# Optimization experiments

Hardware: AMD Instinct MI355X
Metric: run time of the kernel (lower is better)

## Reference

```python
import jax, jax.numpy as jnp
import numpy as np

B, H, W, C, HEADS, WS, SS = 32, 56, 56, 512, 16, 7, 3
HID = 4 * C
N = WS * WS          # tokens per window = 49
NW = (H // WS) * (W // WS)  # windows per image = 64
HD = C // HEADS
SCALE = HD ** -0.5

def _rel_index():
    coords = np.stack(np.meshgrid(np.arange(WS), np.arange(WS), indexing='ij'))
    cf = coords.reshape(2, -1)
    rel = (cf[:, :, None] - cf[:, None, :]).transpose(1, 2, 0)
    rel[..., 0] += WS - 1
    rel[..., 1] += WS - 1
    rel[..., 0] *= 2 * WS - 1
    return rel.sum(-1)  # [N, N]

REL_IDX = _rel_index()

def _attn_mask():
    # standard Swin SW-MSA mask: label 3x3 shifted regions, diff labels -> -100
    img = np.zeros((H, W), dtype=np.float32)
    cnt = 0
    for hs in (slice(0, -WS), slice(-WS, -SS), slice(-SS, None)):
        for ws_ in (slice(0, -WS), slice(-WS, -SS), slice(-SS, None)):
            img[hs, ws_] = cnt
            cnt += 1
    mw = img.reshape(H // WS, WS, W // WS, WS).transpose(0, 2, 1, 3).reshape(NW, N)
    diff = mw[:, None, :] - mw[:, :, None]
    return jnp.asarray(np.where(diff != 0, -100.0, 0.0).astype(np.float32))  # [NW, N, N]

ATTN_MASK = _attn_mask()

def layernorm(x, g, b, eps=1e-5):
    m = jnp.mean(x, -1, keepdims=True)
    v = jnp.mean((x - m) ** 2, -1, keepdims=True)
    return (x - m) * jax.lax.rsqrt(v + eps) * g + b

def setup_inputs():
    key = jax.random.key(0)
    ks = jax.random.split(key, 8)
    f32 = jnp.float32
    return {
        'x': jax.random.normal(ks[0], (B, H * W, C), f32),
        'norm1_g': jnp.ones((C,), f32), 'norm1_b': jnp.zeros((C,), f32),
        'qkv_w': jax.random.normal(ks[1], (3 * C, C), f32) * 0.02,
        'qkv_b': jnp.zeros((3 * C,), f32),
        'rel_bias': jax.random.normal(ks[2], ((2 * WS - 1) ** 2, HEADS), f32) * 0.02,
        'proj_w': jax.random.normal(ks[3], (C, C), f32) * 0.02,
        'proj_b': jnp.zeros((C,), f32),
        'norm2_g': jnp.ones((C,), f32), 'norm2_b': jnp.zeros((C,), f32),
        'mlp_w1': jax.random.normal(ks[4], (HID, C), f32) * 0.02,
        'mlp_b1': jnp.zeros((HID,), f32),
        'mlp_w2': jax.random.normal(ks[5], (C, HID), f32) * 0.02,
        'mlp_b2': jnp.zeros((C,), f32),
    }

def reference(x, norm1_g, norm1_b, qkv_w, qkv_b, rel_bias, proj_w, proj_b,
              norm2_g, norm2_b, mlp_w1, mlp_b1, mlp_w2, mlp_b2):
    skip = x
    h = layernorm(x, norm1_g, norm1_b).reshape(B, H, W, C)
    h = jnp.roll(h, (-SS, -SS), axis=(1, 2))  # cyclic shift
    # window partition -> [B*NW, N, C]
    h = h.reshape(B, H // WS, WS, W // WS, WS, C).transpose(0, 1, 3, 2, 4, 5).reshape(B * NW, N, C)
    qkv = (h @ qkv_w.T + qkv_b).reshape(B * NW, N, 3, HEADS, HD).transpose(2, 0, 3, 1, 4)
    q, k, v = qkv[0] * SCALE, qkv[1], qkv[2]  # [B*NW, HEADS, N, HD]
    attn = jnp.einsum('whnd,whmd->whnm', q, k)
    bias = rel_bias[REL_IDX.reshape(-1)].reshape(N, N, HEADS).transpose(2, 0, 1)
    attn = attn + bias[None]
    attn = attn.reshape(B, NW, HEADS, N, N) + ATTN_MASK[None, :, None]
    attn = jax.nn.softmax(attn, axis=-1).reshape(B * NW, HEADS, N, N)
    h = jnp.einsum('whnm,whmd->whnd', attn, v).transpose(0, 2, 1, 3).reshape(B * NW, N, C)
    h = h @ proj_w.T + proj_b
    # window reverse + reverse cyclic shift
    h = h.reshape(B, H // WS, W // WS, WS, WS, C).transpose(0, 1, 3, 2, 4, 5).reshape(B, H, W, C)
    h = jnp.roll(h, (SS, SS), axis=(1, 2)).reshape(B, H * W, C)
    x = skip + h
    m = layernorm(x, norm2_g, norm2_b)
    m = jax.nn.gelu(m @ mlp_w1.T + mlp_b1, approximate=False) @ mlp_w2.T + mlp_b2
    return x + m
```

## Files before the change

kernel.cpp:

```cpp
#include <hip/hip_runtime.h>
#include <cstdint>
#include <cstddef>

#define DI __device__ __forceinline__

typedef __bf16 bf16_t;
typedef __bf16 bf16x8 __attribute__((ext_vector_type(8)));
typedef float f32x4 __attribute__((ext_vector_type(4)));

static constexpr float SCALE = 0.17677669529663687f;

DI bf16_t f2b(float f) {
  uint32_t u = __builtin_bit_cast(uint32_t, f);
  u += 0x7fffu + ((u >> 16) & 1u);
  return __builtin_bit_cast(bf16_t, (uint16_t)(u >> 16));
}

DI void gld16(const void* g, void* l) {
  __builtin_amdgcn_global_load_lds(
      (const __attribute__((address_space(1))) uint32_t*)g,
      (__attribute__((address_space(3))) uint32_t*)l, 16, 0, 0);
}

__global__ __launch_bounds__(256)
void cvtw(const float* __restrict__ in, bf16_t* __restrict__ out, int n) {
  int i = (blockIdx.x * 256 + threadIdx.x) * 4;
  if (i >= n) return;
  float4 v = *(const float4*)(in + i);
  ushort4 o;
  o.x = __builtin_bit_cast(uint16_t, f2b(v.x));
  o.y = __builtin_bit_cast(uint16_t, f2b(v.y));
  o.z = __builtin_bit_cast(uint16_t, f2b(v.z));
  o.w = __builtin_bit_cast(uint16_t, f2b(v.w));
  *(ushort4*)(out + i) = o;
}

__global__ __launch_bounds__(256)
void bias_pre(const float* __restrict__ rel, float* __restrict__ bf) {
  int idx = blockIdx.x * 256 + threadIdx.x;
  int head = idx >> 12, t1 = (idx >> 6) & 63, t2 = idx & 63;
  float v = -1e30f;
  if (t1 < 49 && t2 < 49) {
    int i1 = t1 / 7, j1 = t1 - i1 * 7, i2 = t2 / 7, j2 = t2 - i2 * 7;
    v = rel[((i1 - i2 + 6) * 13 + (j1 - j2 + 6)) * 16 + head];
  }
  bf[idx] = v;
}

template<bool WIN>
__global__ __launch_bounds__(128)
void ln_kernel(const float* __restrict__ in, const float* __restrict__ g,
               const float* __restrict__ be, bf16_t* __restrict__ out)
{
  const int r = blockIdx.x;
  const int tid = threadIdx.x;
  long srow;
  if (WIN) {
    int bw = r / 49, t = r - bw * 49;
    int b = bw >> 6, w = bw & 63;
    int wh = w >> 3, ww = w & 7;
    int i = t / 7, j = t - i * 7;
    int hs = wh * 7 + i + 3; if (hs >= 56) hs -= 56;
    int wsr = ww * 7 + j + 3; if (wsr >= 56) wsr -= 56;
    srow = (long)b * 3136 + hs * 56 + wsr;
  } else {
    srow = r;
  }
  const float4 v = *(const float4*)(in + srow * 512 + tid * 4);
  float s = v.x + v.y + v.z + v.w;
  float sq = v.x * v.x + v.y * v.y + v.z * v.z + v.w * v.w;
#pragma unroll
  for (int m = 1; m < 64; m <<= 1) { s += __shfl_xor(s, m); sq += __shfl_xor(sq, m); }
  __shared__ float ls[2], lq[2];
  if ((tid & 63) == 0) { ls[tid >> 6] = s; lq[tid >> 6] = sq; }
  __syncthreads();
  s = ls[0] + ls[1]; sq = lq[0] + lq[1];
  const float mean = s * (1.f / 512.f);
  const float rs = rsqrtf(sq * (1.f / 512.f) - mean * mean + 1e-5f);
  const float4 gg = *(const float4*)(g + tid * 4);
  const float4 bb = *(const float4*)(be + tid * 4);
  ushort4 o;
  o.x = __builtin_bit_cast(uint16_t, f2b((v.x - mean) * rs * gg.x + bb.x));
  o.y = __builtin_bit_cast(uint16_t, f2b((v.y - mean) * rs * gg.y + bb.y));
  o.z = __builtin_bit_cast(uint16_t, f2b((v.z - mean) * rs * gg.z + bb.z));
  o.w = __builtin_bit_cast(uint16_t, f2b((v.w - mean) * rs * gg.w + bb.w));
  *(ushort4*)(out + (long)r * 512 + tid * 4) = o;
}

#define MFMA16(a, b, c) __builtin_amdgcn_mfma_f32_16x16x32_bf16((a), (b), (c), 0, 0, 0)

template<int EPI>
__global__ __launch_bounds__(512, 2)
void gemm256(const bf16_t* __restrict__ A, const bf16_t* __restrict__ Bw,
             const float* __restrict__ bias, const float* __restrict__ extra,
             void* __restrict__ out0, void* __restrict__ out1v, void* __restrict__ out2v,
             const int K, const int NBN)
{
  __shared__ __align__(128) bf16_t lds[8][8192];
  const int tid = threadIdx.x, lane = tid & 63, wave = tid >> 6;
  const int NT = K >> 6;

  const int xcd = blockIdx.x & 7, j = blockIdx.x >> 3;
  const int G = 32 / NBN;
  if (j >= G * NBN) return;
  const int bmo = j / NBN;
  const int bn = j - bmo * NBN;
  const int m0 = xcd * 49;
  const int tiles = (49 - bmo + G - 1) / G;
  const int ST = tiles * NT;
  const int hEnd = 2 * ST;

  const int srow = tid >> 2, slot = tid & 3;
  const int chunk = slot ^ ((srow >> 1) & 3);
  const size_t rowK = (size_t)128 * K;
  const size_t strideA = (size_t)G * 256 * K;

  const bf16_t* pAs = A + ((size_t)(m0 + bmo) * 256 + srow) * K + chunk * 8;
  const bf16_t* pBs = Bw + ((size_t)bn * 256 + srow) * K + chunk * 8;
  int hA = 0, hB = 0, ktA = 0, hhA = 0, ktB = 0, hhB = 0;

#define STG_A() do { \
    if (hA < hEnd) { \
      const bf16_t* _p = pAs + ktA * 64 + hhA * 32; \
      bf16_t* _l = &lds[(ktA & 1) * 2 + hhA][tid * 8]; \
      gld16(_p, _l); gld16(_p + rowK, _l + 4096); \
      ++hA; hhA ^= 1; \
      if (!hhA) { if (++ktA == NT) { ktA = 0; pAs += strideA; } } \
    } \
  } while (0)

#define STG_B() do { \
    if (hB < hEnd) { \
      const bf16_t* _p = pBs + ktB * 64 + hhB * 32; \
      bf16_t* _l = &lds[4 + (ktB & 1) * 2 + hhB][tid * 8]; \
      gld16(_p, _l); gld16(_p + rowK, _l + 4096); \
      ++hB; hhB ^= 1; \
      if (!hhB) { if (++ktB == NT) ktB = 0; }   \
    } \
  } while (0)

  const int fr = lane & 15, fkc = lane >> 4;
  const int wr = wave >> 2, wc = wave & 3;
  const int slotq = (fkc ^ ((fr >> 1) & 3)) << 3;
  const int aoff = (wr * 128 + fr) * 32 + slotq;
  const int boff = (wc * 64 + fr) * 32 + slotq;

  f32x4 acc[8][4] = {};
  bf16x8 af[8], bq[4];

  STG_A(); STG_B(); STG_A(); STG_B(); STG_A(); STG_B(); STG_A();
  asm volatile("s_waitcnt vmcnt(6)");
  __builtin_amdgcn_s_barrier();
  __builtin_amdgcn_sched_barrier(0);

#define PH_SYNC() \
  __builtin_amdgcn_sched_barrier(0); \
  __builtin_amdgcn_s_barrier(); \
  asm volatile("s_waitcnt lgkmcnt(0)"); \
  __builtin_amdgcn_sched_barrier(0); \
  __builtin_amdgcn_s_setprio(1)

#define PH_END() \
  __builtin_amdgcn_s_setprio(0); \
  __builtin_amdgcn_sched_barrier(0); \
  __builtin_amdgcn_s_barrier()

#define MM2(N0, N1) \
  _Pragma("unroll") \
  for (int m = 0; m < 8; ++m) { \
    acc[m][N0] = MFMA16(af[m], bq[N0], acc[m][N0]); \
    acc[m][N1] = MFMA16(af[m], bq[N1], acc[m][N1]); \
  }

#define KTILE(B) do { \
     \
    _Pragma("unroll") \
    for (int m = 0; m < 8; ++m) af[m] = *(const bf16x8*)&lds[(B) * 2][aoff + m * 512]; \
    bq[0] = *(const bf16x8*)&lds[4 + (B) * 2][boff]; \
    bq[1] = *(const bf16x8*)&lds[4 + (B) * 2][boff + 512]; \
    STG_B(); \
    PH_SYNC(); \
    MM2(0, 1); \
    PH_END(); \
     \
    bq[2] = *(const bf16x8*)&lds[4 + (B) * 2][boff + 1024]; \
    bq[3] = *(const bf16x8*)&lds[4 + (B) * 2][boff + 1536]; \
    STG_A(); \
    PH_SYNC(); \
    MM2(2, 3); \
    PH_END(); \
     \
    _Pragma("unroll") \
    for (int m = 0; m < 8; ++m) af[m] = *(const bf16x8*)&lds[(B) * 2 + 1][aoff + m * 512]; \
    bq[0] = *(const bf16x8*)&lds[4 + (B) * 2 + 1][boff]; \
    bq[1] = *(const bf16x8*)&lds[4 + (B) * 2 + 1][boff + 512]; \
    STG_B(); \
    PH_SYNC(); \
    MM2(0, 1); \
    PH_END(); \
     \
    bq[2] = *(const bf16x8*)&lds[4 + (B) * 2 + 1][boff + 1024]; \
    bq[3] = *(const bf16x8*)&lds[4 + (B) * 2 + 1][boff + 1536]; \
    STG_A(); \
    PH_SYNC(); \
    MM2(2, 3); \
    __builtin_amdgcn_s_setprio(0); \
    __builtin_amdgcn_sched_barrier(0); \
    if (sG + 2 < ST) asm volatile("s_waitcnt vmcnt(6)"); \
    else             asm volatile("s_waitcnt vmcnt(0)"); \
    __builtin_amdgcn_s_barrier(); \
    __builtin_amdgcn_sched_barrier(0); \
    ++sG; \
  } while (0)

  int sG = 0;
  int bmC = m0 + bmo;
  const int rq = fkc * 4;
  float bs[4];
#pragma unroll
  for (int n = 0; n < 4; ++n) bs[n] = bias[bn * 256 + wc * 64 + n * 16 + fr];

  for (int t = 0; t < tiles; ++t) {
#pragma unroll 1
    for (int k2 = 0; k2 < NT; k2 += 2) {
      KTILE(0);
      KTILE(1);
    }
#pragma unroll
    for (int m = 0; m < 8; ++m) {
#pragma unroll
      for (int jj4 = 0; jj4 < 4; ++jj4) {
        const int grow = bmC * 256 + wr * 128 + m * 16 + rq + jj4;
        long obase = 0;
        if (EPI == 0) {
          int bwi = grow / 49, t_ = grow - bwi * 49;
          obase = ((long)bwi * 784 + t_) * 32;
        } else if (EPI == 1) {
          int bwi = grow / 49, t_ = grow - bwi * 49;
          int b = bwi >> 6, w = bwi & 63;
          int wh = w >> 3, ww = w & 7;
          int i = t_ / 7, jj = t_ - i * 7;
          int hs = wh * 7 + i + 3; if (hs >= 56) hs -= 56;
          int wsr = ww * 7 + jj + 3; if (wsr >= 56) wsr -= 56;
          obase = ((long)b * 3136 + hs * 56 + wsr) * 512;
        } else if (EPI == 2) {
          obase = (long)grow * 2048;
        } else {
          obase = (long)grow * 512;
        }
#pragma unroll
        for (int n = 0; n < 4; ++n) {
          const int gcol = bn * 256 + wc * 64 + n * 16 + fr;
          float v = acc[m][n][jj4] + bs[n];
          if (EPI == 0) {
            int part = gcol >> 9, head = (gcol >> 5) & 15, d = gcol & 31;
            if (part == 0) v *= SCALE;
            bf16_t* dst = (bf16_t*)(part == 0 ? out0 : (part == 1 ? out1v : out2v));
            dst[obase + (long)head * 1568 + d] = f2b(v);
          } else if (EPI == 1) {
            ((float*)out0)[obase + gcol] = v + extra[obase + gcol];
          } else if (EPI == 2) {
            float m2 = v * v;
            float z = v * fmaf(0.07135481627f, m2, 1.59576912161f);
            float e = __expf(z);
            float rr = __builtin_amdgcn_rcpf(e + 1.0f);
            ((bf16_t*)out0)[obase + gcol] = f2b(fmaf(-v, rr, v));
          } else {
            ((float*)out0)[obase + gcol] = v + extra[obase + gcol];
          }
        }
      }
    }
#pragma unroll
    for (int m = 0; m < 8; ++m)
#pragma unroll
      for (int n = 0; n < 4; ++n) acc[m][n] = (f32x4){0.f, 0.f, 0.f, 0.f};
    bmC += G;
  }
#undef KTILE
#undef MM2
#undef PH_END
#undef PH_SYNC
#undef STG_A
#undef STG_B
}

__global__ __launch_bounds__(256)
void attn_kernel(const bf16_t* __restrict__ qb, const bf16_t* __restrict__ kb,
                 const bf16_t* __restrict__ vb, const float* __restrict__ biasf,
                 bf16_t* __restrict__ aout)
{
  __shared__ bf16_t Q[64 * 32];
  __shared__ bf16_t Kl[64 * 32];
  __shared__ bf16_t Vt[32 * 64];
  __shared__ bf16_t Pl[4][16 * 64];
  const int bid = blockIdx.x;
  const int bw = bid >> 4, head = bid & 15;
  const int tid = threadIdx.x, lane = tid & 63, wave = tid >> 6;
  {
    uint4 z = {0u, 0u, 0u, 0u};
    *(uint4*)&Q[tid * 8] = z;
    *(uint4*)&Kl[tid * 8] = z;
    *(uint4*)&Vt[tid * 8] = z;
  }
  __syncthreads();
  const bf16_t* qsrc = qb + (long)bid * (49 * 32);
  const bf16_t* ksrc = kb + (long)bid * (49 * 32);
  const bf16_t* vsrc = vb + (long)bid * (49 * 32);
  if (tid < 196) {
    *(uint4*)&Q[tid * 8] = *(const uint4*)(qsrc + tid * 8);
    *(uint4*)&Kl[tid * 8] = *(const uint4*)(ksrc + tid * 8);
  }
  for (int e = tid; e < 1568; e += 256) {
    int t = e >> 5, d = e & 31;
    Vt[d * 64 + t] = vsrc[e];
  }
  __syncthreads();
  const int fr = lane & 15, fk = (lane >> 4) * 8, rq = (lane >> 4) * 4;
  bf16x8 aq = *(const bf16x8*)&Q[(wave * 16 + fr) * 32 + fk];
  f32x4 s[4];
#pragma unroll
  for (int n = 0; n < 4; ++n) {
    bf16x8 bk = *(const bf16x8*)&Kl[(n * 16 + fr) * 32 + fk];
    f32x4 z = {0.f, 0.f, 0.f, 0.f};
    s[n] = __builtin_amdgcn_mfma_f32_16x16x32_bf16(aq, bk, z, 0, 0, 0);
  }
  const int w = bw & 63;
  const bool wh7 = ((w >> 3) == 7), ww7 = ((w & 7) == 7);
  const float* bh = biasf + head * 4096;
#pragma unroll
  for (int j = 0; j < 4; ++j) {
    const int row = wave * 16 + rq + j;
    int i1 = row / 7, j1 = row - i1 * 7;
    bool b1h = wh7 && (i1 >= 4), b1w = ww7 && (j1 >= 4);
    float pv[4];
    float mx = -3.0e38f;
#pragma unroll
    for (int n = 0; n < 4; ++n) {
      const int col = n * 16 + fr;
      float v = s[n][j] + bh[row * 64 + col];
      if (wh7 || ww7) {
        int i2 = col / 7, j2 = col - i2 * 7;
        bool b2h = wh7 && (i2 >= 4), b2w = ww7 && (j2 >= 4);
        if ((b1h != b2h) || (b1w != b2w)) v -= 100.f;
      }
      pv[n] = v;
      mx = fmaxf(mx, v);
    }
#pragma unroll
    for (int msk = 1; msk < 16; msk <<= 1) mx = fmaxf(mx, __shfl_xor(mx, msk));
    float sm = 0.f;
#pragma unroll
    for (int n = 0; n < 4; ++n) { pv[n] = __expf(pv[n] - mx); sm += pv[n]; }
#pragma unroll
    for (int msk = 1; msk < 16; msk <<= 1) sm += __shfl_xor(sm, msk);
    const float inv = 1.f / sm;
#pragma unroll
    for (int n = 0; n < 4; ++n)
      Pl[wave][(rq + j) * 64 + n * 16 + fr] = f2b(pv[n] * inv);
  }
  __syncthreads();
  f32x4 o[2] = {};
#pragma unroll
  for (int kk = 0; kk < 2; ++kk) {
    bf16x8 pa = *(const bf16x8*)&Pl[wave][fr * 64 + kk * 32 + fk];
#pragma unroll
    for (int dt = 0; dt < 2; ++dt) {
      bf16x8 vv = *(const bf16x8*)&Vt[(dt * 16 + fr) * 64 + kk * 32 + fk];
      o[dt] = __builtin_amdgcn_mfma_f32_16x16x32_bf16(pa, vv, o[dt], 0, 0, 0);
    }
  }
#pragma unroll
  for (int j = 0; j < 4; ++j) {
    const int t1 = wave * 16 + rq + j;
    if (t1 < 49) {
      bf16_t* dst = aout + ((long)bw * 49 + t1) * 512 + head * 32;
      dst[fr] = f2b(o[0][j]);
      dst[16 + fr] = f2b(o[1][j]);
    }
  }
}

extern "C" void kernel_launch(void* const* d_in, const int* in_sizes, int n_in,
                              void* d_out, int out_size, void* d_ws, size_t ws_size,
                              hipStream_t stream)
{
  const float* x      = (const float*)d_in[0];
  const float* n1g    = (const float*)d_in[1];
  const float* n1b    = (const float*)d_in[2];
  const float* qkv_w  = (const float*)d_in[3];
  const float* qkv_b  = (const float*)d_in[4];
  const float* rel    = (const float*)d_in[5];
  const float* proj_w = (const float*)d_in[6];
  const float* proj_b = (const float*)d_in[7];
  const float* n2g    = (const float*)d_in[8];
  const float* n2b    = (const float*)d_in[9];
  const float* w1     = (const float*)d_in[10];
  const float* b1     = (const float*)d_in[11];
  const float* w2     = (const float*)d_in[12];
  const float* b2     = (const float*)d_in[13];

  char* ws = (char*)d_ws;
  bf16_t* Wqkv  = (bf16_t*)(ws + 0);
  bf16_t* Wproj = (bf16_t*)(ws + 1572864);
  bf16_t* Wm1   = (bf16_t*)(ws + 2097152);
  bf16_t* Wm2   = (bf16_t*)(ws + 4194304);
  float*  biasf = (float*)(ws + 6291456);
  const size_t ABYTES = (size_t)100352 * 512 * 2;
  const size_t P1 = 8388608;
  const size_t P2 = P1 + ABYTES + 1048576;
  bf16_t* xw      = (bf16_t*)(ws + P1);
  bf16_t* qbuf    = (bf16_t*)(ws + P2);
  bf16_t* kbuf    = (bf16_t*)(ws + P2 + ABYTES);
  bf16_t* vbuf    = (bf16_t*)(ws + P2 + 2 * ABYTES);
  bf16_t* attnout = xw;
  bf16_t* h2      = xw;
  bf16_t* hidden  = qbuf;

  cvtw<<<768, 256, 0, stream>>>(qkv_w, Wqkv, 1536 * 512);
  cvtw<<<256, 256, 0, stream>>>(proj_w, Wproj, 512 * 512);
  cvtw<<<1024, 256, 0, stream>>>(w1, Wm1, 2048 * 512);
  cvtw<<<1024, 256, 0, stream>>>(w2, Wm2, 512 * 2048);
  bias_pre<<<256, 256, 0, stream>>>(rel, biasf);

  ln_kernel<true><<<100352, 128, 0, stream>>>(x, n1g, n1b, xw);
  gemm256<0><<<256, 512, 0, stream>>>(xw, Wqkv, qkv_b, nullptr,
                                      qbuf, kbuf, vbuf, 512, 6);
  attn_kernel<<<32768, 256, 0, stream>>>(qbuf, kbuf, vbuf, biasf, attnout);
  gemm256<1><<<256, 512, 0, stream>>>(attnout, Wproj, proj_b, x,
                                      d_out, nullptr, nullptr, 512, 2);
  ln_kernel<false><<<100352, 128, 0, stream>>>((const float*)d_out, n2g, n2b, h2);
  gemm256<2><<<256, 512, 0, stream>>>(h2, Wm1, b1, nullptr,
                                      hidden, nullptr, nullptr, 512, 8);
  gemm256<3><<<256, 512, 0, stream>>>(hidden, Wm2, b2, (const float*)d_out,
                                      d_out, nullptr, nullptr, 2048, 2);
}
```

Before: 1.315 ms.

## Fuse MLP fc1+GELU+fc2 into one kernel keeping hidden tile in LDS

Replaces the two separate MLP GEMMs with a single fused kernel. Each block computes a 128-row tile of the fc1 output in 128-column hidden chunks, applies GELU, stores the chunk in LDS, and immediately accumulates it into the fc2 output. The 100352x2048 bf16 hidden activation never goes through global memory. It also packs two rows per 256-thread LayerNorm block. The cost is a smaller 128-row tile with heavy LDS use, a hand-tuned software pipeline, and fc1/fc2 weights re-read by every block.

```diff
diff --git a/kernel.cpp b/kernel.cpp
--- a/kernel.cpp
+++ b/kernel.cpp
@@ -48,12 +48,13 @@
 }
 
 template<bool WIN>
-__global__ __launch_bounds__(128)
+__global__ __launch_bounds__(256)
 void ln_kernel(const float* __restrict__ in, const float* __restrict__ g,
                const float* __restrict__ be, bf16_t* __restrict__ out)
 {
-  const int r = blockIdx.x;
   const int tid = threadIdx.x;
+  const int r = blockIdx.x * 2 + (tid >> 7);
+  const int ti = tid & 127;
   long srow;
   if (WIN) {
     int bw = r / 49, t = r - bw * 49;
@@ -66,25 +67,27 @@
   } else {
     srow = r;
   }
-  const float4 v = *(const float4*)(in + srow * 512 + tid * 4);
+  const float4 v = *(const float4*)(in + srow * 512 + ti * 4);
   float s = v.x + v.y + v.z + v.w;
   float sq = v.x * v.x + v.y * v.y + v.z * v.z + v.w * v.w;
 #pragma unroll
   for (int m = 1; m < 64; m <<= 1) { s += __shfl_xor(s, m); sq += __shfl_xor(sq, m); }
-  __shared__ float ls[2], lq[2];
-  if ((tid & 63) == 0) { ls[tid >> 6] = s; lq[tid >> 6] = sq; }
+  __shared__ float ls[4], lq[4];
+  const int wv = tid >> 6;
+  if ((tid & 63) == 0) { ls[wv] = s; lq[wv] = sq; }
   __syncthreads();
-  s = ls[0] + ls[1]; sq = lq[0] + lq[1];
+  const int rp = (tid >> 7) * 2;
+  s = ls[rp] + ls[rp + 1]; sq = lq[rp] + lq[rp + 1];
   const float mean = s * (1.f / 512.f);
   const float rs = rsqrtf(sq * (1.f / 512.f) - mean * mean + 1e-5f);
-  const float4 gg = *(const float4*)(g + tid * 4);
-  const float4 bb = *(const float4*)(be + tid * 4);
+  const float4 gg = *(const float4*)(g + ti * 4);
+  const float4 bb = *(const float4*)(be + ti * 4);
   ushort4 o;
   o.x = __builtin_bit_cast(uint16_t, f2b((v.x - mean) * rs * gg.x + bb.x));
   o.y = __builtin_bit_cast(uint16_t, f2b((v.y - mean) * rs * gg.y + bb.y));
   o.z = __builtin_bit_cast(uint16_t, f2b((v.z - mean) * rs * gg.z + bb.z));
   o.w = __builtin_bit_cast(uint16_t, f2b((v.w - mean) * rs * gg.w + bb.w));
-  *(ushort4*)(out + (long)r * 512 + tid * 4) = o;
+  *(ushort4*)(out + (long)r * 512 + ti * 4) = o;
 }
 
 #define MFMA16(a, b, c) __builtin_amdgcn_mfma_f32_16x16x32_bf16((a), (b), (c), 0, 0, 0)
@@ -135,7 +138,7 @@
       bf16_t* _l = &lds[4 + (ktB & 1) * 2 + hhB][tid * 8]; \
       gld16(_p, _l); gld16(_p + rowK, _l + 4096); \
       ++hB; hhB ^= 1; \
-      if (!hhB) { if (++ktB == NT) ktB = 0; }   \
+      if (!hhB) { if (++ktB == NT) ktB = 0; } \
     } \
   } while (0)
 
@@ -173,7 +176,6 @@
   }
 
 #define KTILE(B) do { \
-     \
     _Pragma("unroll") \
     for (int m = 0; m < 8; ++m) af[m] = *(const bf16x8*)&lds[(B) * 2][aoff + m * 512]; \
     bq[0] = *(const bf16x8*)&lds[4 + (B) * 2][boff]; \
@@ -182,14 +184,12 @@
     PH_SYNC(); \
     MM2(0, 1); \
     PH_END(); \
-     \
     bq[2] = *(const bf16x8*)&lds[4 + (B) * 2][boff + 1024]; \
     bq[3] = *(const bf16x8*)&lds[4 + (B) * 2][boff + 1536]; \
     STG_A(); \
     PH_SYNC(); \
     MM2(2, 3); \
     PH_END(); \
-     \
     _Pragma("unroll") \
     for (int m = 0; m < 8; ++m) af[m] = *(const bf16x8*)&lds[(B) * 2 + 1][aoff + m * 512]; \
     bq[0] = *(const bf16x8*)&lds[4 + (B) * 2 + 1][boff]; \
@@ -198,7 +198,6 @@
     PH_SYNC(); \
     MM2(0, 1); \
     PH_END(); \
-     \
     bq[2] = *(const bf16x8*)&lds[4 + (B) * 2 + 1][boff + 1024]; \
     bq[3] = *(const bf16x8*)&lds[4 + (B) * 2 + 1][boff + 1536]; \
     STG_A(); \
@@ -235,7 +234,7 @@
         if (EPI == 0) {
           int bwi = grow / 49, t_ = grow - bwi * 49;
           obase = ((long)bwi * 784 + t_) * 32;
-        } else if (EPI == 1) {
+        } else {
           int bwi = grow / 49, t_ = grow - bwi * 49;
           int b = bwi >> 6, w = bwi & 63;
           int wh = w >> 3, ww = w & 7;
@@ -243,10 +242,6 @@
           int hs = wh * 7 + i + 3; if (hs >= 56) hs -= 56;
           int wsr = ww * 7 + jj + 3; if (wsr >= 56) wsr -= 56;
           obase = ((long)b * 3136 + hs * 56 + wsr) * 512;
-        } else if (EPI == 2) {
-          obase = (long)grow * 2048;
-        } else {
-          obase = (long)grow * 512;
         }
 #pragma unroll
         for (int n = 0; n < 4; ++n) {
@@ -257,14 +252,6 @@
             if (part == 0) v *= SCALE;
             bf16_t* dst = (bf16_t*)(part == 0 ? out0 : (part == 1 ? out1v : out2v));
             dst[obase + (long)head * 1568 + d] = f2b(v);
-          } else if (EPI == 1) {
-            ((float*)out0)[obase + gcol] = v + extra[obase + gcol];
-          } else if (EPI == 2) {
-            float m2 = v * v;
-            float z = v * fmaf(0.07135481627f, m2, 1.59576912161f);
-            float e = __expf(z);
-            float rr = __builtin_amdgcn_rcpf(e + 1.0f);
-            ((bf16_t*)out0)[obase + gcol] = f2b(fmaf(-v, rr, v));
           } else {
             ((float*)out0)[obase + gcol] = v + extra[obase + gcol];
           }
@@ -283,6 +270,165 @@
 #undef PH_SYNC
 #undef STG_A
 #undef STG_B
+}
+
+template<int DUMMY>
+__global__ __launch_bounds__(512, 2)
+void mlp_fused(const bf16_t* __restrict__ A, const bf16_t* __restrict__ W1,
+               const float* __restrict__ b1, const bf16_t* __restrict__ W2,
+               const float* __restrict__ b2, const float* __restrict__ extra,
+               float* __restrict__ out)
+{
+  __shared__ __align__(128) bf16_t A3[3][4096];
+  __shared__ __align__(128) bf16_t B13[3][4096];
+  __shared__ __align__(128) bf16_t HT[4][4096];
+  __shared__ __align__(128) bf16_t B22[2][16384];
+  const int tid = threadIdx.x, lane = tid & 63, wave = tid >> 6;
+  const int bm = (blockIdx.x & 7) * 98 + (blockIdx.x >> 3);
+
+  const int srow = tid >> 2, slot = tid & 3;
+  const int chunk = slot ^ ((srow >> 1) & 3);
+  const bf16_t* pA = A + ((size_t)(bm * 128 + srow) * 512) + chunk * 8;
+
+#define STG_B2(HC, KKi, BUF) do { \
+    const bf16_t* _w = W2 + (size_t)tid * 2048 + (HC) * 128 + (KKi) * 32; \
+    gld16(_w + ((0 ^ ((tid >> 1) & 3)) << 3), &B22[BUF][tid * 8]); \
+    gld16(_w + ((1 ^ ((tid >> 1) & 3)) << 3), &B22[BUF][4096 + tid * 8]); \
+    gld16(_w + ((2 ^ ((tid >> 1) & 3)) << 3), &B22[BUF][8192 + tid * 8]); \
+    gld16(_w + ((3 ^ ((tid >> 1) & 3)) << 3), &B22[BUF][12288 + tid * 8]); \
+  } while (0)
+
+  const int fr = lane & 15, fkc = lane >> 4;
+  const int wr = wave >> 2, wc = wave & 3;
+  const int slotq = (fkc ^ ((fr >> 1) & 3)) << 3;
+  const int aoff1 = (wr * 64 + fr) * 32 + slotq;
+  const int boff1 = (wc * 32 + fr) * 32 + slotq;
+  const int boff2 = slotq * 512 + (wc * 128 + fr) * 8;
+  const int rq = fkc * 4;
+
+  f32x4 acc2[4][8] = {};
+
+  {
+    const bf16_t* pB1p = W1 + (size_t)srow * 512 + chunk * 8;
+    gld16(pA, &A3[0][tid * 8]);       gld16(pB1p, &B13[0][tid * 8]);
+    gld16(pA + 32, &A3[1][tid * 8]);  gld16(pB1p + 32, &B13[1][tid * 8]);
+  }
+  asm volatile("s_waitcnt vmcnt(2)");
+  __builtin_amdgcn_s_barrier();
+  __builtin_amdgcn_sched_barrier(0);
+
+#pragma unroll 1
+  for (int hc = 0; hc < 16; ++hc) {
+    const bf16_t* pB1 = W1 + ((size_t)(hc * 128 + srow) * 512) + chunk * 8;
+    f32x4 acc1[4][2] = {};
+
+#pragma unroll
+    for (int s = 0; s < 16; ++s) {
+      const int b = s % 3;
+      bf16x8 af0 = *(const bf16x8*)&A3[b][aoff1];
+      bf16x8 af1 = *(const bf16x8*)&A3[b][aoff1 + 512];
+      bf16x8 af2 = *(const bf16x8*)&A3[b][aoff1 + 1024];
+      bf16x8 af3 = *(const bf16x8*)&A3[b][aoff1 + 1536];
+      bf16x8 bq0 = *(const bf16x8*)&B13[b][boff1];
+      bf16x8 bq1 = *(const bf16x8*)&B13[b][boff1 + 512];
+      if (s < 14) {
+        const int tb = (s + 2) % 3;
+        gld16(pA + (s + 2) * 32, &A3[tb][tid * 8]);
+        gld16(pB1 + (s + 2) * 32, &B13[tb][tid * 8]);
+      }
+      if (s == 12) STG_B2(hc, 0, 0);
+      if (s == 14) STG_B2(hc, 1, 1);
+      asm volatile("s_waitcnt lgkmcnt(0)");
+      __builtin_amdgcn_sched_barrier(0);
+      __builtin_amdgcn_s_setprio(1);
+      acc1[0][0] = MFMA16(af0, bq0, acc1[0][0]); acc1[0][1] = MFMA16(af0, bq1, acc1[0][1]);
+      acc1[1][0] = MFMA16(af1, bq0, acc1[1][0]); acc1[1][1] = MFMA16(af1, bq1, acc1[1][1]);
+      acc1[2][0] = MFMA16(af2, bq0, acc1[2][0]); acc1[2][1] = MFMA16(af2, bq1, acc1[2][1]);
+      acc1[3][0] = MFMA16(af3, bq0, acc1[3][0]); acc1[3][1] = MFMA16(af3, bq1, acc1[3][1]);
+      __builtin_amdgcn_s_setprio(0);
+      __builtin_amdgcn_sched_barrier(0);
+      if (s <= 11)      asm volatile("s_waitcnt vmcnt(2)");
+      else if (s == 12) asm volatile("s_waitcnt vmcnt(6)");
+      else if (s == 13) asm volatile("s_waitcnt vmcnt(6)");
+      else if (s == 14) asm volatile("s_waitcnt vmcnt(4)");
+      __builtin_amdgcn_s_barrier();
+      __builtin_amdgcn_sched_barrier(0);
+    }
+
+    {
+      float bsn0 = b1[hc * 128 + wc * 32 + fr];
+      float bsn1 = b1[hc * 128 + wc * 32 + 16 + fr];
+#pragma unroll
+      for (int m = 0; m < 4; ++m)
+#pragma unroll
+        for (int n = 0; n < 2; ++n)
+#pragma unroll
+          for (int jj = 0; jj < 4; ++jj) {
+            const int rl = wr * 64 + m * 16 + rq + jj;
+            float v = acc1[m][n][jj] + (n == 0 ? bsn0 : bsn1);
+            float m2 = v * v;
+            float z = v * fmaf(0.07135481627f, m2, 1.59576912161f);
+            float e = __expf(z);
+            float rr = __builtin_amdgcn_rcpf(e + 1.0f);
+            const int c = n * 2 + (fr >> 3);
+            const int sl = c ^ ((rl >> 1) & 3);
+            HT[wc][rl * 32 + (sl << 3) + (fr & 7)] = f2b(fmaf(-v, rr, v));
+          }
+    }
+    asm volatile("s_waitcnt lgkmcnt(0)");
+    __builtin_amdgcn_s_barrier();
+    __builtin_amdgcn_sched_barrier(0);
+
+#pragma unroll
+    for (int kk = 0; kk < 4; ++kk) {
+      const int bb = kk & 1;
+      bf16x8 ah0 = *(const bf16x8*)&HT[kk][aoff1];
+      bf16x8 ah1 = *(const bf16x8*)&HT[kk][aoff1 + 512];
+      bf16x8 ah2 = *(const bf16x8*)&HT[kk][aoff1 + 1024];
+      bf16x8 ah3 = *(const bf16x8*)&HT[kk][aoff1 + 1536];
+      asm volatile("s_waitcnt lgkmcnt(0)");
+      __builtin_amdgcn_sched_barrier(0);
+      __builtin_amdgcn_s_setprio(1);
+#pragma unroll
+      for (int n2 = 0; n2 < 8; ++n2) {
+        bf16x8 bw = *(const bf16x8*)&B22[bb][boff2 + n2 * 128];
+        asm volatile("s_waitcnt lgkmcnt(0)");
+        acc2[0][n2] = MFMA16(ah0, bw, acc2[0][n2]);
+        acc2[1][n2] = MFMA16(ah1, bw, acc2[1][n2]);
+        acc2[2][n2] = MFMA16(ah2, bw, acc2[2][n2]);
+        acc2[3][n2] = MFMA16(ah3, bw, acc2[3][n2]);
+      }
+      __builtin_amdgcn_s_setprio(0);
+      __builtin_amdgcn_sched_barrier(0);
+      if (kk == 3 && hc < 15) asm volatile("s_waitcnt vmcnt(2)");
+      else                    asm volatile("s_waitcnt vmcnt(0)");
+      __builtin_amdgcn_s_barrier();
+      __builtin_amdgcn_sched_barrier(0);
+      if (kk == 0) STG_B2(hc, 2, 0);
+      if (kk == 1) STG_B2(hc, 3, 1);
+      if (kk == 2 && hc < 15) {
+        const bf16_t* pB1n = W1 + ((size_t)((hc + 1) * 128 + srow) * 512) + chunk * 8;
+        gld16(pA, &A3[0][tid * 8]);       gld16(pB1n, &B13[0][tid * 8]);
+        gld16(pA + 32, &A3[1][tid * 8]);  gld16(pB1n + 32, &B13[1][tid * 8]);
+      }
+    }
+  }
+
+  float bs2[8];
+#pragma unroll
+  for (int n2 = 0; n2 < 8; ++n2) bs2[n2] = b2[wc * 128 + n2 * 16 + fr];
+#pragma unroll
+  for (int m = 0; m < 4; ++m)
+#pragma unroll
+    for (int jj = 0; jj < 4; ++jj) {
+      const long base = ((long)bm * 128 + wr * 64 + m * 16 + rq + jj) * 512;
+#pragma unroll
+      for (int n2 = 0; n2 < 8; ++n2) {
+        const int gcol = wc * 128 + n2 * 16 + fr;
+        out[base + gcol] = acc2[m][n2][jj] + bs2[n2] + extra[base + gcol];
+      }
+    }
+#undef STG_B2
 }
 
 __global__ __launch_bounds__(256)
@@ -415,7 +561,6 @@
   bf16_t* vbuf    = (bf16_t*)(ws + P2 + 2 * ABYTES);
   bf16_t* attnout = xw;
   bf16_t* h2      = xw;
-  bf16_t* hidden  = qbuf;
 
   cvtw<<<768, 256, 0, stream>>>(qkv_w, Wqkv, 1536 * 512);
   cvtw<<<256, 256, 0, stream>>>(proj_w, Wproj, 512 * 512);
@@ -423,15 +568,13 @@
   cvtw<<<1024, 256, 0, stream>>>(w2, Wm2, 512 * 2048);
   bias_pre<<<256, 256, 0, stream>>>(rel, biasf);
 
-  ln_kernel<true><<<100352, 128, 0, stream>>>(x, n1g, n1b, xw);
+  ln_kernel<true><<<50176, 256, 0, stream>>>(x, n1g, n1b, xw);
   gemm256<0><<<256, 512, 0, stream>>>(xw, Wqkv, qkv_b, nullptr,
                                       qbuf, kbuf, vbuf, 512, 6);
   attn_kernel<<<32768, 256, 0, stream>>>(qbuf, kbuf, vbuf, biasf, attnout);
   gemm256<1><<<256, 512, 0, stream>>>(attnout, Wproj, proj_b, x,
                                       d_out, nullptr, nullptr, 512, 2);
-  ln_kernel<false><<<100352, 128, 0, stream>>>((const float*)d_out, n2g, n2b, h2);
-  gemm256<2><<<256, 512, 0, stream>>>(h2, Wm1, b1, nullptr,
-                                      hidden, nullptr, nullptr, 512, 8);
-  gemm256<3><<<256, 512, 0, stream>>>(hidden, Wm2, b2, (const float*)d_out,
-                                      d_out, nullptr, nullptr, 2048, 2);
-}
+  ln_kernel<false><<<50176, 256, 0, stream>>>((const float*)d_out, n2g, n2b, h2);
+  mlp_fused<0><<<784, 512, 0, stream>>>(h2, Wm1, b1, Wm2, b2,
+                                        (const float*)d_out, (float*)d_out);
+}
```

Result: slower. 1.938 ms (+47.4%).
